# Optimization experiments

Measured on AMD Instinct MI355X. Metric: run time of the kernel, lower is better.

## Reference

```python
import jax, jax.numpy as jnp
import numpy as np

N = 50000
E = 800000
IN_FT = 256
OUT_FT = 64


def setup_inputs() -> dict:
    key = jax.random.key(0)
    k_seq, k_w, k_src, k_dst, k_val = jax.random.split(key, 5)
    seq = jax.random.normal(k_seq, (N, IN_FT), dtype=jnp.float32)
    # xavier_uniform_ for fc.weight [out_ft, in_ft]
    limit = float(np.sqrt(6.0 / (IN_FT + OUT_FT)))
    W = jax.random.uniform(k_w, (OUT_FT, IN_FT), minval=-limit, maxval=limit, dtype=jnp.float32)
    bias = jnp.zeros((OUT_FT,), dtype=jnp.float32)          # bias.data.fill_(0.0)
    alpha = jnp.full((1,), 0.25, dtype=jnp.float32)         # PReLU default init
    edge_src = jax.random.randint(k_src, (E,), 0, N, dtype=jnp.int32)
    edge_dst = jax.random.randint(k_dst, (E,), 0, N, dtype=jnp.int32)
    edge_val = jax.random.uniform(k_val, (E,), dtype=jnp.float32)
    return {"seq": seq, "W": W, "bias": bias, "alpha": alpha,
            "edge_src": edge_src, "edge_dst": edge_dst, "edge_val": edge_val}


def reference(seq, W, bias, alpha, edge_src, edge_dst, edge_val):
    # fc(seq): [N, in_ft] @ [in_ft, out_ft] -> [N, out_ft]
    fts = jnp.einsum('ni,oi->no', seq, W)
    # spmm(adj, fts): gather source features, scale by edge value, scatter-add to dst
    msgs = fts[edge_src] * edge_val[:, None]                # [E, out_ft]
    out = jax.ops.segment_sum(msgs, edge_dst, num_segments=seq.shape[0])
    out = out + bias
    # PReLU with scalar (single-channel) alpha
    return jnp.where(out >= 0, out, alpha * out)
```

## Files before the change

### kernel.cpp

```cpp
#include <hip/hip_runtime.h>
#include <hip/hip_fp16.h>

#define IN_FT 256
#define OUT_FT 64

constexpr int BIN_LOG   = 7;
constexpr int BIN_NODES = 1 << BIN_LOG;
constexpr int MAX_NBIN  = 512;
constexpr int BIN_CAP   = 2560;
constexpr int SC_BLOCKS = 256;

typedef _Float16 half8 __attribute__((ext_vector_type(8)));
typedef float    f32x4 __attribute__((ext_vector_type(4)));

__global__ __launch_bounds__(256) void fused_gemm_scatter(
    const float* __restrict__ seq, const float* __restrict__ W,
    __half* __restrict__ fts, int N, int G,
    const int* __restrict__ src, const int* __restrict__ dst,
    const float* __restrict__ val, int* __restrict__ binCursor,
    int2* __restrict__ binned, int E, int NBIN)
{
    const int t = (int)threadIdx.x;

    if ((int)blockIdx.x >= G) {
        __shared__ int h[MAX_NBIN];
        __shared__ int base[MAX_NBIN];
        const int sb = (int)blockIdx.x - G;
        for (int i = t; i < NBIN; i += 256) h[i] = 0;
        __syncthreads();
        const int chunk = (E + SC_BLOCKS - 1) / SC_BLOCKS;
        const int s0 = sb * chunk;
        const int e0 = min(s0 + chunk, E);
        for (int i = s0 + t; i < e0; i += 256) atomicAdd(&h[dst[i] >> BIN_LOG], 1);
        __syncthreads();
        for (int i = t; i < NBIN; i += 256) {
            int c = h[i];
            base[i] = c ? atomicAdd(&binCursor[i], c) : 0;
            h[i] = 0;
        }
        __syncthreads();
        for (int i = s0 + t; i < e0; i += 256) {
            int d = dst[i];
            int b = d >> BIN_LOG;
            int pos = base[b] + atomicAdd(&h[b], 1);
            if (pos < BIN_CAP) {
                int2 pr;
                pr.x = src[i] | ((d & (BIN_NODES - 1)) << 16);
                pr.y = __float_as_int(val[i]);
                binned[(size_t)b * BIN_CAP + pos] = pr;
            }
        }
        return;
    }

    __shared__ half8 Wh[4 * 8 * 64];

#pragma unroll
    for (int i = 0; i < 8; ++i) {
        int item = i * 256 + t;
        int l  = item & 63;
        int kc = (item >> 6) & 7;
        int nt = item >> 9;
        int m  = l & 15;
        int q  = l >> 4;
        const float* wp = W + (size_t)(nt * 16 + m) * IN_FT + kc * 32 + q * 8;
        float4 w0 = *(const float4*)wp;
        float4 w1 = *(const float4*)(wp + 4);
        half8 hh;
        hh[0] = (_Float16)w0.x; hh[1] = (_Float16)w0.y;
        hh[2] = (_Float16)w0.z; hh[3] = (_Float16)w0.w;
        hh[4] = (_Float16)w1.x; hh[5] = (_Float16)w1.y;
        hh[6] = (_Float16)w1.z; hh[7] = (_Float16)w1.w;
        Wh[item] = hh;
    }
    __syncthreads();

    const int wave = t >> 6;
    const int l    = t & 63;
    int nodeBase = (int)blockIdx.x * 64 + wave * 16;
    const bool active = (nodeBase < N);
    if (nodeBase > N - 16) nodeBase = N - 16;
    const int m = l & 15;
    const int q = l >> 4;
    const float* ap = seq + (size_t)(nodeBase + m) * IN_FT + q * 8;

    f32x4 acc0 = {0.f, 0.f, 0.f, 0.f};
    f32x4 acc1 = {0.f, 0.f, 0.f, 0.f};
    f32x4 acc2 = {0.f, 0.f, 0.f, 0.f};
    f32x4 acc3 = {0.f, 0.f, 0.f, 0.f};

    float4 a0 = *(const float4*)(ap);
    float4 a1 = *(const float4*)(ap + 4);

#pragma unroll
    for (int kc = 0; kc < 8; ++kc) {
        float4 c0 = a0, c1 = a1;
        if (kc < 7) {
            a0 = *(const float4*)(ap + (kc + 1) * 32);
            a1 = *(const float4*)(ap + (kc + 1) * 32 + 4);
        }
        half8 af;
        af[0] = (_Float16)c0.x; af[1] = (_Float16)c0.y;
        af[2] = (_Float16)c0.z; af[3] = (_Float16)c0.w;
        af[4] = (_Float16)c1.x; af[5] = (_Float16)c1.y;
        af[6] = (_Float16)c1.z; af[7] = (_Float16)c1.w;

        half8 b0 = Wh[(0 * 8 + kc) * 64 + l];
        half8 b1 = Wh[(1 * 8 + kc) * 64 + l];
        half8 b2 = Wh[(2 * 8 + kc) * 64 + l];
        half8 b3 = Wh[(3 * 8 + kc) * 64 + l];
        acc0 = __builtin_amdgcn_mfma_f32_16x16x32_f16(af, b0, acc0, 0, 0, 0);
        acc1 = __builtin_amdgcn_mfma_f32_16x16x32_f16(af, b1, acc1, 0, 0, 0);
        acc2 = __builtin_amdgcn_mfma_f32_16x16x32_f16(af, b2, acc2, 0, 0, 0);
        acc3 = __builtin_amdgcn_mfma_f32_16x16x32_f16(af, b3, acc3, 0, 0, 0);
    }

    if (active) {
#pragma unroll
        for (int r = 0; r < 4; ++r) {
            int node = nodeBase + q * 4 + r;
            __half* op = fts + (size_t)node * OUT_FT + m;
            op[0]  = __float2half(acc0[r]);
            op[16] = __float2half(acc1[r]);
            op[32] = __float2half(acc2[r]);
            op[48] = __float2half(acc3[r]);
        }
    }
}

__device__ __forceinline__ int block_excl_scan_256(int v, int t) {
    int lane = t & 63, wv = t >> 6;
    int incl = v;
#pragma unroll
    for (int d = 1; d < 64; d <<= 1) {
        int u = __shfl_up(incl, d, 64);
        if (lane >= d) incl += u;
    }
    __shared__ int wsum[4];
    if (lane == 63) wsum[wv] = incl;
    __syncthreads();
    int woff = 0;
    for (int i = 0; i < wv; ++i) woff += wsum[i];
    return woff + incl - v;
}

__global__ __launch_bounds__(256) void bin_sort(
    const int2* __restrict__ binned, const int* __restrict__ binCursor,
    int* __restrict__ offsets, unsigned int* __restrict__ pairs,
    int N, int E, int NBIN)
{
    __shared__ int cnt[BIN_NODES];
    __shared__ int cur[BIN_NODES];
    __shared__ int red[4];
    const int b = (int)blockIdx.x;
    const int t = (int)threadIdx.x;
    const int lane = t & 63, wv = t >> 6;
    const int nodeBase = b << BIN_LOG;

    int s = 0;
    for (int i = t; i < b; i += 256) s += binCursor[i];
#pragma unroll
    for (int d = 32; d >= 1; d >>= 1) s += __shfl_down(s, d, 64);
    if (lane == 0) red[wv] = s;
    if (t < BIN_NODES) cnt[t] = 0;
    __syncthreads();
    const int start = red[0] + red[1] + red[2] + red[3];
    const int nrec  = min(binCursor[b], BIN_CAP);
    const int2* rec = binned + (size_t)b * BIN_CAP;

    for (int i = t; i < nrec; i += 256) atomicAdd(&cnt[rec[i].x >> 16], 1);
    __syncthreads();
    int v = (t < BIN_NODES) ? cnt[t] : 0;
    int excl = block_excl_scan_256(v, t);
    if (t < BIN_NODES) {
        cur[t] = start + excl;
        int node = nodeBase + t;
        if (node < N) offsets[node] = start + excl;
    }
    if (b == NBIN - 1 && t == 0) offsets[N] = E;
    __syncthreads();
    for (int i = t; i < nrec; i += 256) {
        int2 pr = rec[i];
        int pos = atomicAdd(&cur[pr.x >> 16], 1);
        float vv = __int_as_float(pr.y);
        pairs[pos] = (unsigned int)(pr.x & 0xFFFF) |
                     ((unsigned int)__half_as_ushort(__float2half_rn(vv)) << 16);
    }
}

__global__ __launch_bounds__(256) void gather_kernel(
    const __half* __restrict__ fts, const int* __restrict__ offsets,
    const unsigned int* __restrict__ pairs,
    const float* __restrict__ bias, const float* __restrict__ alpha,
    float* __restrict__ out, int N)
{
    int gtid = (int)blockIdx.x * 256 + (int)threadIdx.x;
    int node = gtid >> 6;
    int lane = gtid & 63;
    if (node >= N) return;
    int e0 = offsets[node];
    int deg = offsets[node + 1] - e0;
    float acc = 0.f;

    for (int base = 0; base < deg; base += 64) {
        int cnt = min(64, deg - base);
        unsigned int pReg = 0;
        if (lane < cnt) pReg = pairs[e0 + base + lane];
        int j = 0;
        for (; j + 8 <= cnt; j += 8) {
            unsigned int p[8];
            float f[8];
#pragma unroll
            for (int k = 0; k < 8; ++k)
                p[k] = (unsigned int)__shfl((int)pReg, j + k, 64);
#pragma unroll
            for (int k = 0; k < 8; ++k)
                f[k] = __half2float(fts[(size_t)(p[k] & 0xFFFFu) * OUT_FT + lane]);
#pragma unroll
            for (int k = 0; k < 8; ++k) {
                float v = __half2float(__ushort_as_half((unsigned short)(p[k] >> 16)));
                acc = fmaf(f[k], v, acc);
            }
        }
        for (; j < cnt; ++j) {
            unsigned int pj = (unsigned int)__shfl((int)pReg, j, 64);
            float fj = __half2float(fts[(size_t)(pj & 0xFFFFu) * OUT_FT + lane]);
            float vj = __half2float(__ushort_as_half((unsigned short)(pj >> 16)));
            acc = fmaf(fj, vj, acc);
        }
    }
    float o = acc + bias[lane];
    float a = alpha[0];
    out[(size_t)node * OUT_FT + lane] = (o >= 0.f) ? o : a * o;
}

extern "C" void kernel_launch(void* const* d_in, const int* in_sizes, int n_in,
                              void* d_out, int out_size, void* d_ws, size_t ws_size,
                              hipStream_t stream) {
    const float* seq      = (const float*)d_in[0];
    const float* W        = (const float*)d_in[1];
    const float* bias     = (const float*)d_in[2];
    const float* alpha    = (const float*)d_in[3];
    const int*   edge_src = (const int*)d_in[4];
    const int*   edge_dst = (const int*)d_in[5];
    const float* edge_val = (const float*)d_in[6];
    float* out = (float*)d_out;

    const int N    = in_sizes[0] / IN_FT;
    const int E    = in_sizes[4];
    const int NBIN = (N + BIN_NODES - 1) >> BIN_LOG;

    size_t off = 0;
    auto take = [&](size_t bytes) -> char* {
        char* p = (char*)d_ws + off;
        off += (bytes + 255) & ~(size_t)255;
        return p;
    };
    __half*       fts       = (__half*)take((size_t)N * OUT_FT * sizeof(__half));
    int*          binCursor = (int*)take((size_t)NBIN * sizeof(int));
    int*          offsets   = (int*)take(((size_t)N + 1) * sizeof(int));
    int2*         binned    = (int2*)take((size_t)NBIN * BIN_CAP * sizeof(int2));
    unsigned int* pairs     = (unsigned int*)take((size_t)E * sizeof(unsigned int));
    (void)ws_size;

    hipMemsetAsync(binCursor, 0, (size_t)NBIN * sizeof(int), stream);

    const int G = (N + 63) / 64;
    fused_gemm_scatter<<<G + SC_BLOCKS, 256, 0, stream>>>(
        seq, W, fts, N, G, edge_src, edge_dst, edge_val,
        binCursor, binned, E, NBIN);

    bin_sort<<<NBIN, 256, 0, stream>>>(
        binned, binCursor, offsets, pairs, N, E, NBIN);
    gather_kernel<<<((size_t)N * 64 + 255) / 256, 256, 0, stream>>>(
        fts, offsets, pairs, bias, alpha, out, N);
}
```

Baseline: 160.2 us.

## Replace CSR sort and gather with per-bin LDS atomic reduction; precompute fp16 W

Drops the bin_sort and gather kernels. A new bin_reduce kernel accumulates messages for each 64-node bin straight into a shared-memory tile with LDS float atomics, then applies bias and PReLU and writes the output. Bins shrink to 64 nodes with a smaller capacity. The fp16 conversion of W moves into a small separate kernel so each GEMM block reads it from global memory instead of rebuilding it in LDS. This removes the CSR offsets and pairs passes and one launch, at the cost of LDS atomic contention and a lower overflow cap per bin (1536 against about 1024 expected edges). Summation order now varies from run to run.

Measured after the change: 471.1 us. 2.94x slower.

```diff
diff --git a/kernel.cpp b/kernel.cpp
--- a/kernel.cpp
+++ b/kernel.cpp
@@ -4,17 +4,37 @@
 #define IN_FT 256
 #define OUT_FT 64
 
-constexpr int BIN_LOG   = 7;
+constexpr int BIN_LOG   = 6;
 constexpr int BIN_NODES = 1 << BIN_LOG;
-constexpr int MAX_NBIN  = 512;
-constexpr int BIN_CAP   = 2560;
+constexpr int MAX_NBIN  = 1024;
+constexpr int BIN_CAP   = 1536;
 constexpr int SC_BLOCKS = 256;
 
 typedef _Float16 half8 __attribute__((ext_vector_type(8)));
 typedef float    f32x4 __attribute__((ext_vector_type(4)));
 
+__global__ __launch_bounds__(256) void wconv_kernel(
+    const float* __restrict__ W, half8* __restrict__ Wh)
+{
+    int item = (int)blockIdx.x * 256 + (int)threadIdx.x;
+    int l  = item & 63;
+    int kc = (item >> 6) & 7;
+    int nt = item >> 9;
+    int m  = l & 15;
+    int q  = l >> 4;
+    const float* wp = W + (size_t)(nt * 16 + m) * IN_FT + kc * 32 + q * 8;
+    float4 w0 = *(const float4*)wp;
+    float4 w1 = *(const float4*)(wp + 4);
+    half8 hh;
+    hh[0] = (_Float16)w0.x; hh[1] = (_Float16)w0.y;
+    hh[2] = (_Float16)w0.z; hh[3] = (_Float16)w0.w;
+    hh[4] = (_Float16)w1.x; hh[5] = (_Float16)w1.y;
+    hh[6] = (_Float16)w1.z; hh[7] = (_Float16)w1.w;
+    Wh[item] = hh;
+}
+
 __global__ __launch_bounds__(256) void fused_gemm_scatter(
-    const float* __restrict__ seq, const float* __restrict__ W,
+    const float* __restrict__ seq, const half8* __restrict__ WhG,
     __half* __restrict__ fts, int N, int G,
     const int* __restrict__ src, const int* __restrict__ dst,
     const float* __restrict__ val, int* __restrict__ binCursor,
@@ -53,28 +73,6 @@
         return;
     }
 
-    __shared__ half8 Wh[4 * 8 * 64];
-
-#pragma unroll
-    for (int i = 0; i < 8; ++i) {
-        int item = i * 256 + t;
-        int l  = item & 63;
-        int kc = (item >> 6) & 7;
-        int nt = item >> 9;
-        int m  = l & 15;
-        int q  = l >> 4;
-        const float* wp = W + (size_t)(nt * 16 + m) * IN_FT + kc * 32 + q * 8;
-        float4 w0 = *(const float4*)wp;
-        float4 w1 = *(const float4*)(wp + 4);
-        half8 hh;
-        hh[0] = (_Float16)w0.x; hh[1] = (_Float16)w0.y;
-        hh[2] = (_Float16)w0.z; hh[3] = (_Float16)w0.w;
-        hh[4] = (_Float16)w1.x; hh[5] = (_Float16)w1.y;
-        hh[6] = (_Float16)w1.z; hh[7] = (_Float16)w1.w;
-        Wh[item] = hh;
-    }
-    __syncthreads();
-
     const int wave = t >> 6;
     const int l    = t & 63;
     int nodeBase = (int)blockIdx.x * 64 + wave * 16;
@@ -105,10 +103,10 @@
         af[4] = (_Float16)c1.x; af[5] = (_Float16)c1.y;
         af[6] = (_Float16)c1.z; af[7] = (_Float16)c1.w;
 
-        half8 b0 = Wh[(0 * 8 + kc) * 64 + l];
-        half8 b1 = Wh[(1 * 8 + kc) * 64 + l];
-        half8 b2 = Wh[(2 * 8 + kc) * 64 + l];
-        half8 b3 = Wh[(3 * 8 + kc) * 64 + l];
+        half8 b0 = WhG[(0 * 8 + kc) * 64 + l];
+        half8 b1 = WhG[(1 * 8 + kc) * 64 + l];
+        half8 b2 = WhG[(2 * 8 + kc) * 64 + l];
+        half8 b3 = WhG[(3 * 8 + kc) * 64 + l];
         acc0 = __builtin_amdgcn_mfma_f32_16x16x32_f16(af, b0, acc0, 0, 0, 0);
         acc1 = __builtin_amdgcn_mfma_f32_16x16x32_f16(af, b1, acc1, 0, 0, 0);
         acc2 = __builtin_amdgcn_mfma_f32_16x16x32_f16(af, b2, acc2, 0, 0, 0);
@@ -128,110 +126,66 @@
     }
 }
 
-__device__ __forceinline__ int block_excl_scan_256(int v, int t) {
-    int lane = t & 63, wv = t >> 6;
-    int incl = v;
-#pragma unroll
-    for (int d = 1; d < 64; d <<= 1) {
-        int u = __shfl_up(incl, d, 64);
-        if (lane >= d) incl += u;
-    }
-    __shared__ int wsum[4];
-    if (lane == 63) wsum[wv] = incl;
+__global__ __launch_bounds__(256) void bin_reduce(
+    const int2* __restrict__ binned, const int* __restrict__ binCursor,
+    const __half* __restrict__ fts, const float* __restrict__ bias,
+    const float* __restrict__ alpha, float* __restrict__ out, int N)
+{
+    __shared__ float accum[BIN_NODES * OUT_FT];
+    const int b    = (int)blockIdx.x;
+    const int t    = (int)threadIdx.x;
+    const int lane = t & 63;
+    const int wv   = t >> 6;
+
+    f32x4* a4 = (f32x4*)accum;
+#pragma unroll
+    for (int i = 0; i < (BIN_NODES * OUT_FT / 4) / 256; ++i)
+        a4[i * 256 + t] = (f32x4){0.f, 0.f, 0.f, 0.f};
     __syncthreads();
-    int woff = 0;
-    for (int i = 0; i < wv; ++i) woff += wsum[i];
-    return woff + incl - v;
-}
-
-__global__ __launch_bounds__(256) void bin_sort(
-    const int2* __restrict__ binned, const int* __restrict__ binCursor,
-    int* __restrict__ offsets, unsigned int* __restrict__ pairs,
-    int N, int E, int NBIN)
-{
-    __shared__ int cnt[BIN_NODES];
-    __shared__ int cur[BIN_NODES];
-    __shared__ int red[4];
-    const int b = (int)blockIdx.x;
-    const int t = (int)threadIdx.x;
-    const int lane = t & 63, wv = t >> 6;
-    const int nodeBase = b << BIN_LOG;
-
-    int s = 0;
-    for (int i = t; i < b; i += 256) s += binCursor[i];
-#pragma unroll
-    for (int d = 32; d >= 1; d >>= 1) s += __shfl_down(s, d, 64);
-    if (lane == 0) red[wv] = s;
-    if (t < BIN_NODES) cnt[t] = 0;
+
+    const int nrec = min(binCursor[b], BIN_CAP);
+    const int2* rec = binned + (size_t)b * BIN_CAP;
+
+    for (int i = wv * 8; i < nrec; i += 32) {
+        if (i + 8 <= nrec) {
+            int2 pr[8];
+#pragma unroll
+            for (int k = 0; k < 8; ++k) pr[k] = rec[i + k];
+            float f[8];
+#pragma unroll
+            for (int k = 0; k < 8; ++k)
+                f[k] = __half2float(fts[(size_t)(pr[k].x & 0xFFFF) * OUT_FT + lane]);
+#pragma unroll
+            for (int k = 0; k < 8; ++k)
+                atomicAdd(&accum[(pr[k].x >> 16) * OUT_FT + lane],
+                          f[k] * __int_as_float(pr[k].y));
+        } else {
+            for (int k = 0; i + k < nrec; ++k) {
+                int2 pr = rec[i + k];
+                float fv = __half2float(fts[(size_t)(pr.x & 0xFFFF) * OUT_FT + lane]);
+                atomicAdd(&accum[(pr.x >> 16) * OUT_FT + lane],
+                          fv * __int_as_float(pr.y));
+            }
+        }
+    }
     __syncthreads();
-    const int start = red[0] + red[1] + red[2] + red[3];
-    const int nrec  = min(binCursor[b], BIN_CAP);
-    const int2* rec = binned + (size_t)b * BIN_CAP;
-
-    for (int i = t; i < nrec; i += 256) atomicAdd(&cnt[rec[i].x >> 16], 1);
-    __syncthreads();
-    int v = (t < BIN_NODES) ? cnt[t] : 0;
-    int excl = block_excl_scan_256(v, t);
-    if (t < BIN_NODES) {
-        cur[t] = start + excl;
-        int node = nodeBase + t;
-        if (node < N) offsets[node] = start + excl;
-    }
-    if (b == NBIN - 1 && t == 0) offsets[N] = E;
-    __syncthreads();
-    for (int i = t; i < nrec; i += 256) {
-        int2 pr = rec[i];
-        int pos = atomicAdd(&cur[pr.x >> 16], 1);
-        float vv = __int_as_float(pr.y);
-        pairs[pos] = (unsigned int)(pr.x & 0xFFFF) |
-                     ((unsigned int)__half_as_ushort(__float2half_rn(vv)) << 16);
-    }
-}
-
-__global__ __launch_bounds__(256) void gather_kernel(
-    const __half* __restrict__ fts, const int* __restrict__ offsets,
-    const unsigned int* __restrict__ pairs,
-    const float* __restrict__ bias, const float* __restrict__ alpha,
-    float* __restrict__ out, int N)
-{
-    int gtid = (int)blockIdx.x * 256 + (int)threadIdx.x;
-    int node = gtid >> 6;
-    int lane = gtid & 63;
-    if (node >= N) return;
-    int e0 = offsets[node];
-    int deg = offsets[node + 1] - e0;
-    float acc = 0.f;
-
-    for (int base = 0; base < deg; base += 64) {
-        int cnt = min(64, deg - base);
-        unsigned int pReg = 0;
-        if (lane < cnt) pReg = pairs[e0 + base + lane];
-        int j = 0;
-        for (; j + 8 <= cnt; j += 8) {
-            unsigned int p[8];
-            float f[8];
-#pragma unroll
-            for (int k = 0; k < 8; ++k)
-                p[k] = (unsigned int)__shfl((int)pReg, j + k, 64);
-#pragma unroll
-            for (int k = 0; k < 8; ++k)
-                f[k] = __half2float(fts[(size_t)(p[k] & 0xFFFFu) * OUT_FT + lane]);
-#pragma unroll
-            for (int k = 0; k < 8; ++k) {
-                float v = __half2float(__ushort_as_half((unsigned short)(p[k] >> 16)));
-                acc = fmaf(f[k], v, acc);
+
+    const float a = alpha[0];
+    for (int i = t; i < BIN_NODES * (OUT_FT / 4); i += 256) {
+        int row  = i >> 4;
+        int c    = (i & 15) << 2;
+        int node = (b << BIN_LOG) + row;
+        if (node < N) {
+            f32x4 v = *(f32x4*)&accum[row * OUT_FT + c];
+            f32x4 o;
+#pragma unroll
+            for (int j = 0; j < 4; ++j) {
+                float x = v[j] + bias[c + j];
+                o[j] = (x >= 0.f) ? x : a * x;
             }
-        }
-        for (; j < cnt; ++j) {
-            unsigned int pj = (unsigned int)__shfl((int)pReg, j, 64);
-            float fj = __half2float(fts[(size_t)(pj & 0xFFFFu) * OUT_FT + lane]);
-            float vj = __half2float(__ushort_as_half((unsigned short)(pj >> 16)));
-            acc = fmaf(fj, vj, acc);
-        }
-    }
-    float o = acc + bias[lane];
-    float a = alpha[0];
-    out[(size_t)node * OUT_FT + lane] = (o >= 0.f) ? o : a * o;
+            *(f32x4*)(out + (size_t)node * OUT_FT + c) = o;
+        }
+    }
 }
 
 extern "C" void kernel_launch(void* const* d_in, const int* in_sizes, int n_in,
@@ -256,22 +210,21 @@
         off += (bytes + 255) & ~(size_t)255;
         return p;
     };
-    __half*       fts       = (__half*)take((size_t)N * OUT_FT * sizeof(__half));
-    int*          binCursor = (int*)take((size_t)NBIN * sizeof(int));
-    int*          offsets   = (int*)take(((size_t)N + 1) * sizeof(int));
-    int2*         binned    = (int2*)take((size_t)NBIN * BIN_CAP * sizeof(int2));
-    unsigned int* pairs     = (unsigned int*)take((size_t)E * sizeof(unsigned int));
+    __half* fts       = (__half*)take((size_t)N * OUT_FT * sizeof(__half));
+    int*    binCursor = (int*)take((size_t)NBIN * sizeof(int));
+    half8*  Wh        = (half8*)take((size_t)4 * 8 * 64 * sizeof(half8));
+    int2*   binned    = (int2*)take((size_t)NBIN * BIN_CAP * sizeof(int2));
     (void)ws_size;
 
     hipMemsetAsync(binCursor, 0, (size_t)NBIN * sizeof(int), stream);
+
+    wconv_kernel<<<8, 256, 0, stream>>>(W, Wh);
 
     const int G = (N + 63) / 64;
     fused_gemm_scatter<<<G + SC_BLOCKS, 256, 0, stream>>>(
-        seq, W, fts, N, G, edge_src, edge_dst, edge_val,
+        seq, Wh, fts, N, G, edge_src, edge_dst, edge_val,
         binCursor, binned, E, NBIN);
 
-    bin_sort<<<NBIN, 256, 0, stream>>>(
-        binned, binCursor, offsets, pairs, N, E, NBIN);
-    gather_kernel<<<((size_t)N * 64 + 255) / 256, 256, 0, stream>>>(
-        fts, offsets, pairs, bias, alpha, out, N);
-}
+    bin_reduce<<<NBIN, 256, 0, stream>>>(
+        binned, binCursor, fts, bias, alpha, out, N);
+}
```
